# Kernel tuning notes

Measured on AMD Instinct MI355X. Metric: run time of the kernel, lower is better.

The kernel has to match this reference:

```python
import jax, jax.numpy as jnp
import numpy as np
import math

D_MODEL = 1024
N_HEADS = 16
D_K = D_MODEL // N_HEADS
THRESH = 0.1  # attention probs below this are zeroed


def setup_inputs() -> dict:
    key = jax.random.key(0)
    ks = jax.random.split(key, 9)
    B, S, D = 2, 2048, D_MODEL
    scale = 1.0 / math.sqrt(D)
    x = jax.random.normal(ks[0], (B, S, D), dtype=jnp.float32)
    Wq = jax.random.normal(ks[1], (D, D), dtype=jnp.float32) * scale
    bq = jax.random.normal(ks[2], (D,), dtype=jnp.float32) * 0.01
    Wk = jax.random.normal(ks[3], (D, D), dtype=jnp.float32) * scale
    bk = jax.random.normal(ks[4], (D,), dtype=jnp.float32) * 0.01
    Wv = jax.random.normal(ks[5], (D, D), dtype=jnp.float32) * scale
    bv = jax.random.normal(ks[6], (D,), dtype=jnp.float32) * 0.01
    Wo = jax.random.normal(ks[7], (D, D), dtype=jnp.float32) * scale
    bo = jax.random.normal(ks[8], (D,), dtype=jnp.float32) * 0.01
    return {"x": x, "Wq": Wq, "bq": bq, "Wk": Wk, "bk": bk,
            "Wv": Wv, "bv": bv, "Wo": Wo, "bo": bo}


def _split_heads(t):
    B, S, D = t.shape
    return t.reshape(B, S, N_HEADS, D_K).transpose(0, 2, 1, 3)  # [B,H,S,dk]


def reference(x, Wq, bq, Wk, bk, Wv, bv, Wo, bo):
    # torch nn.Linear: y = x @ W.T + b
    q = _split_heads(x @ Wq.T + bq)
    k = _split_heads(x @ Wk.T + bk)
    v = _split_heads(x @ Wv.T + bv)
    scores = jnp.einsum('bhqd,bhkd->bhqk', q, k) / math.sqrt(D_K)
    probs = jax.nn.softmax(scores, axis=-1)          # full unmasked softmax (returned)
    keep = probs >= THRESH                            # ~low_attention_mask
    probs_model = jnp.where(keep, probs, 0.0)        # masked_fill; dropout is identity in eval
    ctx = jnp.einsum('bhqk,bhkd->bhqd', probs_model, v)
    B, H, S, dk = ctx.shape
    merged = ctx.transpose(0, 2, 1, 3).reshape(B, S, H * dk)
    out = merged @ Wo.T + bo
    attention_sum = probs.sum(axis=1)                # [B,S,S] sum over heads
    attention_mask = keep.astype(jnp.float32).sum(axis=1)  # [B,S,S]
    return (out, attention_sum, attention_mask)
```

## Files before the change

kernel.cpp:

```cpp
#include <hip/hip_runtime.h>

#define SDIM 2048
#define DDIM 1024
#define NH 16
#define DK 64
#define NB 2
#define MROWS (NB * SDIM)
#define MAXEV 65536
#define EXPC 0.18033688011112f
#define L01 -3.3219281f

typedef _Float16 f16x8 __attribute__((ext_vector_type(8)));
typedef _Float16 f16x4 __attribute__((ext_vector_type(4)));
typedef float f32x4 __attribute__((ext_vector_type(4)));

__device__ __forceinline__ void ld_lds16(const _Float16* g, _Float16* l) {
  __builtin_amdgcn_global_load_lds(
      (const __attribute__((address_space(1))) void*)g,
      (__attribute__((address_space(3))) void*)l, 16, 0, 0);
}

__global__ __launch_bounds__(256) void cvt_f16(
    const float* __restrict__ x, const float* __restrict__ wq,
    const float* __restrict__ wk, const float* __restrict__ wv,
    _Float16* __restrict__ xh, _Float16* __restrict__ wqh,
    _Float16* __restrict__ wkh, _Float16* __restrict__ wvh) {
  int i = blockIdx.x * 256 + threadIdx.x;
  const float* src;
  _Float16* dst;
  int off;
  if (i < 1048576) {
    src = x; dst = xh; off = i;
  } else if (i < 1310720) {
    src = wq; dst = wqh; off = i - 1048576;
  } else if (i < 1572864) {
    src = wk; dst = wkh; off = i - 1310720;
  } else {
    src = wv; dst = wvh; off = i - 1572864;
  }
  float4 v = ((const float4*)src)[off];
  f16x4 h;
  h[0] = (_Float16)v.x; h[1] = (_Float16)v.y;
  h[2] = (_Float16)v.z; h[3] = (_Float16)v.w;
  ((f16x4*)dst)[off] = h;
}

__global__ __launch_bounds__(256, 2) void proj_gemm(
    const _Float16* __restrict__ xh, const _Float16* __restrict__ Wqh,
    const _Float16* __restrict__ Wkh, const _Float16* __restrict__ Wvh,
    const float* __restrict__ bq, const float* __restrict__ bk,
    const float* __restrict__ bv, _Float16* __restrict__ Qo,
    _Float16* __restrict__ Ko, float* __restrict__ Vo) {
  __shared__ _Float16 sA[128 * 64];
  __shared__ _Float16 sB[128 * 64];
  const int t = threadIdx.x;
  const int lane = t & 63, wv = t >> 6;
  const int lr = lane & 15, quad = lane >> 4;
  const int wm = wv >> 1, wn = wv & 1;
  const int m0 = blockIdx.y * 128, n0 = blockIdx.x * 128;
  const int z = blockIdx.z;
  const _Float16* Bp = z == 0 ? Wqh : (z == 1 ? Wkh : Wvh);
  const float* bias = z == 0 ? bq : (z == 1 ? bk : bv);

  const int strow = t >> 3;
  const int stchunk = t & 7;
  const int stsrc = (stchunk ^ (strow & 7)) * 8;

  f32x4 acc[4][4];
#pragma unroll
  for (int i = 0; i < 4; ++i)
#pragma unroll
    for (int j = 0; j < 4; ++j) acc[i][j] = (f32x4){0.f, 0.f, 0.f, 0.f};

  for (int k0 = 0; k0 < DDIM; k0 += 64) {
    __syncthreads();
#pragma unroll
    for (int i = 0; i < 4; ++i) {
      const int row = i * 32 + strow;
      ld_lds16(&xh[(size_t)(m0 + row) * DDIM + k0 + stsrc],
               &sA[row * 64 + stchunk * 8]);
      ld_lds16(&Bp[(size_t)(n0 + row) * DDIM + k0 + stsrc],
               &sB[row * 64 + stchunk * 8]);
    }
    __syncthreads();
    f16x8 af[4][2], bf[4][2];
#pragma unroll
    for (int i = 0; i < 4; ++i)
#pragma unroll
      for (int kk = 0; kk < 2; ++kk) {
        const int ph = ((kk * 4 + quad) ^ (lr & 7)) * 8;
        af[i][kk] = *(const f16x8*)&sA[(wm * 64 + i * 16 + lr) * 64 + ph];
        bf[i][kk] = *(const f16x8*)&sB[(wn * 64 + i * 16 + lr) * 64 + ph];
      }
#pragma unroll
    for (int kk = 0; kk < 2; ++kk)
#pragma unroll
      for (int i = 0; i < 4; ++i)
#pragma unroll
        for (int j = 0; j < 4; ++j)
          acc[i][j] = __builtin_amdgcn_mfma_f32_16x16x32_f16(
              af[i][kk], bf[j][kk], acc[i][j], 0, 0, 0);
  }
#pragma unroll
  for (int j = 0; j < 4; ++j) {
    const int ng = n0 + wn * 64 + j * 16 + lr;
    const float bvv = bias[ng];
    const int h = ng >> 6, d = ng & 63;
#pragma unroll
    for (int i = 0; i < 4; ++i) {
#pragma unroll
      for (int r = 0; r < 4; ++r) {
        const int mg = m0 + wm * 64 + i * 16 + quad * 4 + r;
        const int b = mg >> 11, s = mg & 2047;
        const float o = acc[i][j][r] + bvv;
        const size_t off = ((size_t)(b * NH + h) * SDIM + s) * DK + d;
        if (z == 0)
          Qo[off] = (_Float16)(o * EXPC);
        else if (z == 1)
          Ko[off] = (_Float16)o;
        else
          Vo[off] = o;
      }
    }
  }
}

__global__ __launch_bounds__(256) void attn_denom(const _Float16* __restrict__ Q,
                                                  const _Float16* __restrict__ K,
                                                  float* __restrict__ laOut) {
  __shared__ _Float16 KdA[128 * 64];
  __shared__ _Float16 KdB[128 * 64];
  const int t = threadIdx.x;
  const int lane = t & 63, wave = t >> 6;
  const int quad = lane >> 4, lr = lane & 15;
  const int q0 = blockIdx.x * 64;
  const int bh = blockIdx.y;
  const _Float16* Qh = Q + (size_t)bh * SDIM * DK;
  const _Float16* Kh = K + (size_t)bh * SDIM * DK;
  const size_t qoff = (size_t)(q0 + wave * 16 + lr) * DK + quad * 8;
  const f16x8 aq0 = *(const f16x8*)&Qh[qoff];
  const f16x8 aq1 = *(const f16x8*)&Qh[qoff + 32];
  const int strow = t >> 3, stchunk = t & 7;
  const int stsrc = (stchunk ^ (strow & 7)) * 8;
  const int ph0 = (quad ^ (lr & 7)) * 8;
  const int ph1 = ((4 + quad) ^ (lr & 7)) * 8;

#define STAGE_DN(KT, BUF)                                                  \
  {                                                                        \
    _Pragma("unroll") for (int i = 0; i < 4; ++i)                          \
        ld_lds16(&Kh[(size_t)((KT)*128 + i * 32 + strow) * DK + stsrc],    \
                 &BUF[(i * 32 + strow) * 64 + stchunk * 8]);               \
  }

#define COMPUTE_DN(BUF)                                                    \
  _Pragma("unroll") for (int c = 0; c < 8; ++c) {                          \
    f16x8 b0 = *(const f16x8*)&BUF[(c * 16 + lr) * 64 + ph0];              \
    f16x8 b1 = *(const f16x8*)&BUF[(c * 16 + lr) * 64 + ph1];              \
    f32x4 acc = {0.f, 0.f, 0.f, 0.f};                                      \
    acc = __builtin_amdgcn_mfma_f32_16x16x32_f16(aq0, b0, acc, 0, 0, 0);   \
    acc = __builtin_amdgcn_mfma_f32_16x16x32_f16(aq1, b1, acc, 0, 0, 0);   \
    _Pragma("unroll") for (int r = 0; r < 4; ++r)                          \
        dsum[r] += __builtin_amdgcn_exp2f(acc[r]);                         \
  }

  float dsum[4] = {0.f, 0.f, 0.f, 0.f};
  STAGE_DN(0, KdA);
#pragma unroll 1
  for (int kt = 0; kt < 16; kt += 2) {
    __syncthreads();
    STAGE_DN(kt + 1, KdB);
    COMPUTE_DN(KdA);
    __syncthreads();
    if (kt + 2 < 16) STAGE_DN(kt + 2, KdA);
    COMPUTE_DN(KdB);
  }
#pragma unroll
  for (int m = 1; m < 16; m <<= 1)
#pragma unroll
    for (int r = 0; r < 4; ++r)
      dsum[r] += __shfl_xor(dsum[r], m, 64);
  if (lr == 0) {
#pragma unroll
    for (int r = 0; r < 4; ++r)
      laOut[(size_t)bh * SDIM + q0 + wave * 16 + quad * 4 + r] =
          -__builtin_amdgcn_logf(dsum[r]);
  }
#undef STAGE_DN
#undef COMPUTE_DN
}

__global__ __launch_bounds__(256) void attn_pass2(
    const _Float16* __restrict__ Q, const _Float16* __restrict__ K,
    const float* __restrict__ la, float* __restrict__ attSum,
    float* __restrict__ attMask, float4* __restrict__ ev,
    int* __restrict__ ecnt) {
  __shared__ _Float16 KbufA[2 * 4096];
  __shared__ _Float16 KbufB[2 * 4096];
  const int t = threadIdx.x;
  const int lane = t & 63, wave = t >> 6;
  const int quad = lane >> 4, lr = lane & 15;
  const int k0 = blockIdx.x * 64;
  const int q0 = blockIdx.y * 64;
  const int b = blockIdx.z;
  const int strow = t >> 3, stchunk = t & 7;
  const int stsrc = (stchunk ^ (strow & 7)) * 8;
  const int ph0 = (quad ^ (lr & 7)) * 8;
  const int ph1 = ((4 + quad) ^ (lr & 7)) * 8;

  const size_t qbase = ((size_t)(b * NH) * SDIM + q0 + wave * 16 + lr) * DK;
  const size_t dbase = (size_t)(b * NH) * SDIM + q0 + wave * 16 + quad * 4;
  const size_t hstep = (size_t)SDIM * DK;

  float asum[4][4] = {};
  float amask[4][4] = {};
  float mx = -1e30f;

  f16x8 a0[2], a1[2];
  float4 lav[2];

#define STAGE_P2(HP, BUF)                                                    \
  {                                                                          \
    _Pragma("unroll") for (int hh = 0; hh < 2; ++hh) {                       \
      const _Float16* Kp =                                                   \
          K + (size_t)(b * NH + 2 * (HP) + hh) * hstep + (size_t)k0 * DK;    \
      _Pragma("unroll") for (int i = 0; i < 2; ++i)                          \
          ld_lds16(&Kp[(size_t)(i * 32 + strow) * DK + stsrc],               \
                   &BUF[hh * 4096 + (i * 32 + strow) * 64 + stchunk * 8]);   \
    }                                                                        \
  }

#define LOADQ_P2(HP)                                                         \
  {                                                                          \
    _Pragma("unroll") for (int hh = 0; hh < 2; ++hh) {                       \
      const size_t ho = (size_t)(2 * (HP) + hh) * hstep;                     \
      a0[hh] = *(const f16x8*)&Q[qbase + ho + quad * 8];                     \
      a1[hh] = *(const f16x8*)&Q[qbase + ho + 32 + quad * 8];                \
      lav[hh] = *(const float4*)&la[dbase + (size_t)(2 * (HP) + hh) * SDIM]; \
    }                                                                        \
  }

#define COMPUTE_P2(BUF)                                                      \
  _Pragma("unroll") for (int hh = 0; hh < 2; ++hh) {                         \
    const _Float16* Ksh = &BUF[hh * 4096];                                   \
    const float lar[4] = {lav[hh].x, lav[hh].y, lav[hh].z, lav[hh].w};       \
    _Pragma("unroll") for (int c = 0; c < 4; ++c) {                          \
      f16x8 b0 = *(const f16x8*)&Ksh[(c * 16 + lr) * 64 + ph0];              \
      f16x8 b1 = *(const f16x8*)&Ksh[(c * 16 + lr) * 64 + ph1];              \
      f32x4 acc = {0.f, 0.f, 0.f, 0.f};                                      \
      acc = __builtin_amdgcn_mfma_f32_16x16x32_f16(a0[hh], b0, acc, 0, 0, 0);\
      acc = __builtin_amdgcn_mfma_f32_16x16x32_f16(a1[hh], b1, acc, 0, 0, 0);\
      _Pragma("unroll") for (int r = 0; r < 4; ++r) {                        \
        const float arg = acc[r] + lar[r];                                   \
        mx = fmaxf(mx, arg);                                                 \
        asum[c][r] += __builtin_amdgcn_exp2f(arg);                           \
      }                                                                      \
    }                                                                        \
  }

  STAGE_P2(0, KbufA);
  LOADQ_P2(0);
#pragma unroll 1
  for (int hp = 0; hp < 8; hp += 2) {
    __syncthreads();
    STAGE_P2(hp + 1, KbufB);
    COMPUTE_P2(KbufA);
    LOADQ_P2(hp + 1);
    __syncthreads();
    if (hp + 2 < 8) STAGE_P2(hp + 2, KbufA);
    COMPUTE_P2(KbufB);
    if (hp + 2 < 8) LOADQ_P2(hp + 2);
  }
#undef STAGE_P2
#undef LOADQ_P2
#undef COMPUTE_P2

  if (__any(mx >= L01)) {
#pragma unroll 1
    for (int h = 0; h < NH; ++h) {
      const _Float16* Kp =
          K + (size_t)(b * NH + h) * hstep + (size_t)k0 * DK;
      const size_t ho = (size_t)h * hstep;
      const f16x8 aq0 = *(const f16x8*)&Q[qbase + ho + quad * 8];
      const f16x8 aq1 = *(const f16x8*)&Q[qbase + ho + 32 + quad * 8];
      const float4 l4 = *(const float4*)&la[dbase + (size_t)h * SDIM];
      const float lar[4] = {l4.x, l4.y, l4.z, l4.w};
#pragma unroll 1
      for (int c = 0; c < 4; ++c) {
        const f16x8 b0 = *(const f16x8*)&Kp[(c * 16 + lr) * DK + quad * 8];
        const f16x8 b1 = *(const f16x8*)&Kp[(c * 16 + lr) * DK + 32 + quad * 8];
        f32x4 acc = {0.f, 0.f, 0.f, 0.f};
        acc = __builtin_amdgcn_mfma_f32_16x16x32_f16(aq0, b0, acc, 0, 0, 0);
        acc = __builtin_amdgcn_mfma_f32_16x16x32_f16(aq1, b1, acc, 0, 0, 0);
#pragma unroll 1
        for (int r = 0; r < 4; ++r) {
          const float p = __builtin_amdgcn_exp2f(acc[r] + lar[r]);
          if (p >= 0.1f) {
            amask[c][r] += 1.0f;
            int idx = atomicAdd(ecnt, 1);
            if (idx < MAXEV)
              ev[idx] = make_float4(
                  __int_as_float(b * NH + h),
                  __int_as_float(q0 + wave * 16 + quad * 4 + r),
                  __int_as_float(k0 + c * 16 + lr), p);
          }
        }
      }
    }
  }
#pragma unroll
  for (int c = 0; c < 4; ++c)
#pragma unroll
    for (int r = 0; r < 4; ++r) {
      const size_t row = (size_t)(b * SDIM) + q0 + wave * 16 + quad * 4 + r;
      const size_t col = (size_t)k0 + c * 16 + lr;
      __builtin_nontemporal_store(asum[c][r], &attSum[row * SDIM + col]);
      __builtin_nontemporal_store(amask[c][r], &attMask[row * SDIM + col]);
    }
}

__global__ __launch_bounds__(64) void apply_events(
    const float4* __restrict__ ev, const int* __restrict__ ecnt,
    const float* __restrict__ V, float* __restrict__ merged,
    int* __restrict__ flags) {
  int n = *ecnt;
  if (n > MAXEV) n = MAXEV;
  const int d = threadIdx.x;
  for (int e = blockIdx.x; e < n; e += gridDim.x) {
    float4 r = ev[e];
    int bh = __float_as_int(r.x);
    int q = __float_as_int(r.y);
    int kc = __float_as_int(r.z);
    float p = r.w;
    int b = bh >> 4, h = bh & 15;
    atomicAdd(&merged[((size_t)(b * SDIM + q)) * DDIM + h * DK + d],
              p * V[((size_t)bh * SDIM + kc) * DK + d]);
    if (d == 0) flags[b * SDIM + q] = 1;
  }
}

__global__ __launch_bounds__(256) void out_gemm(const float* __restrict__ A,
                                                const float* __restrict__ W,
                                                const float* __restrict__ bias,
                                                float* __restrict__ out,
                                                const int* __restrict__ flags) {
  __shared__ float As[16][68];
  __shared__ float Ws[16][68];
  __shared__ int anyF;
  const int t = threadIdx.x;
  const int tx = t & 15, ty = t >> 4;
  const int m0 = blockIdx.y * 64;
  const int n0 = blockIdx.x * 64;
  if (t == 0) anyF = 0;
  __syncthreads();
  if (t < 64 && flags[m0 + t]) anyF = 1;
  __syncthreads();
  const int nb = n0 + tx * 4;
  const float4 bv = *(const float4*)&bias[nb];
  if (!anyF) {
#pragma unroll
    for (int r = 0; r < 4; ++r)
      *(float4*)&out[(size_t)(m0 + ty * 4 + r) * DDIM + nb] = bv;
    return;
  }
  const int lr = t >> 2;
  const int lc = (t & 3) * 4;
  float acc[4][4] = {};
  for (int k0 = 0; k0 < DDIM; k0 += 16) {
    __syncthreads();
    float4 av = *(const float4*)&A[(size_t)(m0 + lr) * DDIM + k0 + lc];
    float4 wv = *(const float4*)&W[(size_t)(n0 + lr) * DDIM + k0 + lc];
    As[lc + 0][lr] = av.x; As[lc + 1][lr] = av.y;
    As[lc + 2][lr] = av.z; As[lc + 3][lr] = av.w;
    Ws[lc + 0][lr] = wv.x; Ws[lc + 1][lr] = wv.y;
    Ws[lc + 2][lr] = wv.z; Ws[lc + 3][lr] = wv.w;
    __syncthreads();
#pragma unroll
    for (int kk = 0; kk < 16; ++kk) {
      float4 a4 = *(const float4*)&As[kk][ty * 4];
      float4 b4 = *(const float4*)&Ws[kk][tx * 4];
      const float a[4] = {a4.x, a4.y, a4.z, a4.w};
      const float b[4] = {b4.x, b4.y, b4.z, b4.w};
#pragma unroll
      for (int r = 0; r < 4; ++r)
#pragma unroll
        for (int c = 0; c < 4; ++c)
          acc[r][c] = fmaf(a[r], b[c], acc[r][c]);
    }
  }
#pragma unroll
  for (int r = 0; r < 4; ++r) {
    float4 o;
    o.x = acc[r][0] + bv.x;
    o.y = acc[r][1] + bv.y;
    o.z = acc[r][2] + bv.z;
    o.w = acc[r][3] + bv.w;
    *(float4*)&out[(size_t)(m0 + ty * 4 + r) * DDIM + nb] = o;
  }
}

extern "C" void kernel_launch(void* const* d_in, const int* in_sizes, int n_in,
                              void* d_out, int out_size, void* d_ws,
                              size_t ws_size, hipStream_t stream) {
  const float* x = (const float*)d_in[0];
  const float* Wq = (const float*)d_in[1];
  const float* bq = (const float*)d_in[2];
  const float* Wk = (const float*)d_in[3];
  const float* bk = (const float*)d_in[4];
  const float* Wv = (const float*)d_in[5];
  const float* bv = (const float*)d_in[6];
  const float* Wo = (const float*)d_in[7];
  const float* bo = (const float*)d_in[8];

  float* out = (float*)d_out;
  float* attSum = out + (size_t)MROWS * DDIM;
  float* attMask = attSum + (size_t)NB * SDIM * SDIM;

  char* ws = (char*)d_ws;
  const size_t bigF = (size_t)MROWS * DDIM * sizeof(float);
  const size_t bigH = (size_t)MROWS * DDIM * sizeof(_Float16);
  const size_t wH = (size_t)DDIM * DDIM * sizeof(_Float16);
  _Float16* Qh = (_Float16*)ws;  ws += bigH;
  _Float16* Kh = (_Float16*)ws;  ws += bigH;
  float* V = (float*)ws;         ws += bigF;
  float* merged = (float*)ws;    ws += bigF;
  _Float16* xh = (_Float16*)ws;  ws += bigH;
  _Float16* Wqh = (_Float16*)ws; ws += wH;
  _Float16* Wkh = (_Float16*)ws; ws += wH;
  _Float16* Wvh = (_Float16*)ws; ws += wH;
  float* laBuf = (float*)ws;     ws += (size_t)NB * NH * SDIM * sizeof(float);
  float4* ev = (float4*)ws;      ws += (size_t)MAXEV * sizeof(float4);
  int* flags = (int*)ws;         ws += (size_t)MROWS * sizeof(int);
  int* ecnt = (int*)ws;          ws += 16;

  hipMemsetAsync(merged, 0, bigF, stream);
  hipMemsetAsync(flags, 0, (size_t)MROWS * sizeof(int), stream);
  hipMemsetAsync(ecnt, 0, 16, stream);

  dim3 blk(256);
  cvt_f16<<<dim3(7168), blk, 0, stream>>>(x, Wq, Wk, Wv, xh, Wqh, Wkh, Wvh);
  proj_gemm<<<dim3(8, 32, 3), blk, 0, stream>>>(xh, Wqh, Wkh, Wvh, bq, bk, bv,
                                                Qh, Kh, V);
  attn_denom<<<dim3(32, 32), blk, 0, stream>>>(Qh, Kh, laBuf);
  attn_pass2<<<dim3(32, 32, 2), blk, 0, stream>>>(Qh, Kh, laBuf, attSum,
                                                  attMask, ev, ecnt);
  apply_events<<<dim3(256), dim3(64), 0, stream>>>(ev, ecnt, V, merged, flags);
  out_gemm<<<dim3(16, 64), blk, 0, stream>>>(merged, Wo, bo, out, flags);
}
```

Baseline: 256.3 us.

## Shrink LDS tiles and add occupancy bounds in attention denominator and pass2

attn_denom now stages 64-row K tiles instead of 128, running twice as many loop iterations, and pass2 stages one head per buffer instead of a pair. This cuts shared memory per block, and launch bounds of 8 and 6 blocks per CU are added so more blocks can be resident. Pass2 also prefetches the next head's Q and log-denominator into separate registers before computing the current head, and tracks the max per row to shorten the dependency chain. The trade is more barriers per unit of work and possible register spills under the tighter bounds.

```diff
diff --git a/kernel.cpp b/kernel.cpp
--- a/kernel.cpp
+++ b/kernel.cpp
@@ -125,11 +125,11 @@
   }
 }
 
-__global__ __launch_bounds__(256) void attn_denom(const _Float16* __restrict__ Q,
-                                                  const _Float16* __restrict__ K,
-                                                  float* __restrict__ laOut) {
-  __shared__ _Float16 KdA[128 * 64];
-  __shared__ _Float16 KdB[128 * 64];
+__global__ __launch_bounds__(256, 8) void attn_denom(
+    const _Float16* __restrict__ Q, const _Float16* __restrict__ K,
+    float* __restrict__ laOut) {
+  __shared__ _Float16 KdA[64 * 64];
+  __shared__ _Float16 KdB[64 * 64];
   const int t = threadIdx.x;
   const int lane = t & 63, wave = t >> 6;
   const int quad = lane >> 4, lr = lane & 15;
@@ -147,31 +147,31 @@
 
 #define STAGE_DN(KT, BUF)                                                  \
   {                                                                        \
-    _Pragma("unroll") for (int i = 0; i < 4; ++i)                          \
-        ld_lds16(&Kh[(size_t)((KT)*128 + i * 32 + strow) * DK + stsrc],    \
+    _Pragma("unroll") for (int i = 0; i < 2; ++i)                          \
+        ld_lds16(&Kh[(size_t)((KT)*64 + i * 32 + strow) * DK + stsrc],     \
                  &BUF[(i * 32 + strow) * 64 + stchunk * 8]);               \
   }
 
-#define COMPUTE_DN(BUF)                                                    \
-  _Pragma("unroll") for (int c = 0; c < 8; ++c) {                          \
-    f16x8 b0 = *(const f16x8*)&BUF[(c * 16 + lr) * 64 + ph0];              \
-    f16x8 b1 = *(const f16x8*)&BUF[(c * 16 + lr) * 64 + ph1];              \
-    f32x4 acc = {0.f, 0.f, 0.f, 0.f};                                      \
-    acc = __builtin_amdgcn_mfma_f32_16x16x32_f16(aq0, b0, acc, 0, 0, 0);   \
-    acc = __builtin_amdgcn_mfma_f32_16x16x32_f16(aq1, b1, acc, 0, 0, 0);   \
-    _Pragma("unroll") for (int r = 0; r < 4; ++r)                          \
-        dsum[r] += __builtin_amdgcn_exp2f(acc[r]);                         \
+#define COMPUTE_DN(BUF)                                                   \
+  _Pragma("unroll") for (int c = 0; c < 4; ++c) {                         \
+    f16x8 b0 = *(const f16x8*)&BUF[(c * 16 + lr) * 64 + ph0];             \
+    f16x8 b1 = *(const f16x8*)&BUF[(c * 16 + lr) * 64 + ph1];             \
+    f32x4 acc = {0.f, 0.f, 0.f, 0.f};                                     \
+    acc = __builtin_amdgcn_mfma_f32_16x16x32_f16(aq0, b0, acc, 0, 0, 0);  \
+    acc = __builtin_amdgcn_mfma_f32_16x16x32_f16(aq1, b1, acc, 0, 0, 0);  \
+    _Pragma("unroll") for (int r = 0; r < 4; ++r)                         \
+        dsum[r] += __builtin_amdgcn_exp2f(acc[r]);                        \
   }
 
   float dsum[4] = {0.f, 0.f, 0.f, 0.f};
   STAGE_DN(0, KdA);
 #pragma unroll 1
-  for (int kt = 0; kt < 16; kt += 2) {
+  for (int kt = 0; kt < 32; kt += 2) {
     __syncthreads();
     STAGE_DN(kt + 1, KdB);
     COMPUTE_DN(KdA);
     __syncthreads();
-    if (kt + 2 < 16) STAGE_DN(kt + 2, KdA);
+    if (kt + 2 < 32) STAGE_DN(kt + 2, KdA);
     COMPUTE_DN(KdB);
   }
 #pragma unroll
@@ -189,13 +189,13 @@
 #undef COMPUTE_DN
 }
 
-__global__ __launch_bounds__(256) void attn_pass2(
+__global__ __launch_bounds__(256, 6) void attn_pass2(
     const _Float16* __restrict__ Q, const _Float16* __restrict__ K,
     const float* __restrict__ la, float* __restrict__ attSum,
     float* __restrict__ attMask, float4* __restrict__ ev,
     int* __restrict__ ecnt) {
-  __shared__ _Float16 KbufA[2 * 4096];
-  __shared__ _Float16 KbufB[2 * 4096];
+  __shared__ _Float16 KbufA[64 * 64];
+  __shared__ _Float16 KbufB[64 * 64];
   const int t = threadIdx.x;
   const int lane = t & 63, wave = t >> 6;
   const int quad = lane >> 4, lr = lane & 15;
@@ -213,67 +213,66 @@
 
   float asum[4][4] = {};
   float amask[4][4] = {};
-  float mx = -1e30f;
-
-  f16x8 a0[2], a1[2];
-  float4 lav[2];
-
-#define STAGE_P2(HP, BUF)                                                    \
+  float mxr[4] = {-1e30f, -1e30f, -1e30f, -1e30f};
+
+  f16x8 aq0c, aq1c, aq0n, aq1n;
+  float4 lavc, lavn;
+
+#define STAGE_H(H, BUF)                                                      \
   {                                                                          \
-    _Pragma("unroll") for (int hh = 0; hh < 2; ++hh) {                       \
-      const _Float16* Kp =                                                   \
-          K + (size_t)(b * NH + 2 * (HP) + hh) * hstep + (size_t)k0 * DK;    \
-      _Pragma("unroll") for (int i = 0; i < 2; ++i)                          \
-          ld_lds16(&Kp[(size_t)(i * 32 + strow) * DK + stsrc],               \
-                   &BUF[hh * 4096 + (i * 32 + strow) * 64 + stchunk * 8]);   \
-    }                                                                        \
-  }
-
-#define LOADQ_P2(HP)                                                         \
+    const _Float16* Kp =                                                     \
+        K + (size_t)(b * NH + (H)) * hstep + (size_t)k0 * DK;                \
+    _Pragma("unroll") for (int i = 0; i < 2; ++i)                            \
+        ld_lds16(&Kp[(size_t)(i * 32 + strow) * DK + stsrc],                 \
+                 &BUF[(i * 32 + strow) * 64 + stchunk * 8]);                 \
+  }
+
+#define LOADQ_H(H, A0, A1, LV)                                               \
   {                                                                          \
-    _Pragma("unroll") for (int hh = 0; hh < 2; ++hh) {                       \
-      const size_t ho = (size_t)(2 * (HP) + hh) * hstep;                     \
-      a0[hh] = *(const f16x8*)&Q[qbase + ho + quad * 8];                     \
-      a1[hh] = *(const f16x8*)&Q[qbase + ho + 32 + quad * 8];                \
-      lav[hh] = *(const float4*)&la[dbase + (size_t)(2 * (HP) + hh) * SDIM]; \
-    }                                                                        \
-  }
-
-#define COMPUTE_P2(BUF)                                                      \
-  _Pragma("unroll") for (int hh = 0; hh < 2; ++hh) {                         \
-    const _Float16* Ksh = &BUF[hh * 4096];                                   \
-    const float lar[4] = {lav[hh].x, lav[hh].y, lav[hh].z, lav[hh].w};       \
+    const size_t ho = (size_t)(H)*hstep;                                     \
+    A0 = *(const f16x8*)&Q[qbase + ho + quad * 8];                           \
+    A1 = *(const f16x8*)&Q[qbase + ho + 32 + quad * 8];                      \
+    LV = *(const float4*)&la[dbase + (size_t)(H)*SDIM];                      \
+  }
+
+#define COMPUTE_H(BUF, A0, A1, LV)                                           \
+  {                                                                          \
+    const float lar[4] = {LV.x, LV.y, LV.z, LV.w};                           \
     _Pragma("unroll") for (int c = 0; c < 4; ++c) {                          \
-      f16x8 b0 = *(const f16x8*)&Ksh[(c * 16 + lr) * 64 + ph0];              \
-      f16x8 b1 = *(const f16x8*)&Ksh[(c * 16 + lr) * 64 + ph1];              \
+      f16x8 b0 = *(const f16x8*)&BUF[(c * 16 + lr) * 64 + ph0];              \
+      f16x8 b1 = *(const f16x8*)&BUF[(c * 16 + lr) * 64 + ph1];              \
       f32x4 acc = {0.f, 0.f, 0.f, 0.f};                                      \
-      acc = __builtin_amdgcn_mfma_f32_16x16x32_f16(a0[hh], b0, acc, 0, 0, 0);\
-      acc = __builtin_amdgcn_mfma_f32_16x16x32_f16(a1[hh], b1, acc, 0, 0, 0);\
+      acc = __builtin_amdgcn_mfma_f32_16x16x32_f16(A0, b0, acc, 0, 0, 0);    \
+      acc = __builtin_amdgcn_mfma_f32_16x16x32_f16(A1, b1, acc, 0, 0, 0);    \
       _Pragma("unroll") for (int r = 0; r < 4; ++r) {                        \
         const float arg = acc[r] + lar[r];                                   \
-        mx = fmaxf(mx, arg);                                                 \
+        mxr[r] = fmaxf(mxr[r], arg);                                         \
         asum[c][r] += __builtin_amdgcn_exp2f(arg);                           \
       }                                                                      \
     }                                                                        \
   }
 
-  STAGE_P2(0, KbufA);
-  LOADQ_P2(0);
+  STAGE_H(0, KbufA);
+  LOADQ_H(0, aq0c, aq1c, lavc);
 #pragma unroll 1
-  for (int hp = 0; hp < 8; hp += 2) {
-    __syncthreads();
-    STAGE_P2(hp + 1, KbufB);
-    COMPUTE_P2(KbufA);
-    LOADQ_P2(hp + 1);
-    __syncthreads();
-    if (hp + 2 < 8) STAGE_P2(hp + 2, KbufA);
-    COMPUTE_P2(KbufB);
-    if (hp + 2 < 8) LOADQ_P2(hp + 2);
-  }
-#undef STAGE_P2
-#undef LOADQ_P2
-#undef COMPUTE_P2
-
+  for (int h = 0; h < NH; h += 2) {
+    __syncthreads();
+    STAGE_H(h + 1, KbufB);
+    LOADQ_H(h + 1, aq0n, aq1n, lavn);
+    COMPUTE_H(KbufA, aq0c, aq1c, lavc);
+    __syncthreads();
+    if (h + 2 < NH) {
+      STAGE_H(h + 2, KbufA);
+      LOADQ_H(h + 2, aq0c, aq1c, lavc);
+    }
+    COMPUTE_H(KbufB, aq0n, aq1n, lavn);
+  }
+#undef STAGE_H
+#undef LOADQ_H
+#undef COMPUTE_H
+
+  const float mx =
+      fmaxf(fmaxf(mxr[0], mxr[1]), fmaxf(mxr[2], mxr[3]));
   if (__any(mx >= L01)) {
 #pragma unroll 1
     for (int h = 0; h < NH; ++h) {
```

After: 301.0 us. 1.17x slower.
